# Performance work log

Hardware: AMD Instinct MI355X
Metric: run time of the kernel (lower is better)

## Reference

```python
import jax, jax.numpy as jnp
import numpy as np

DIM = 256
HEADS = 8
NX = NY = 48
RNG = 5
MAX_IDX = (RNG + 1) ** 2  # 36, padding token


def _make_tokens(nx, ny, rng):
    # Half-symmetric tokenization of 2D relative positions (Learnable_rel_pos_embedding.tokenize)
    xm, ym = np.meshgrid(np.arange(nx), np.arange(ny), indexing='ij')
    xm, ym = xm.ravel(), ym.ravel()
    dx = xm[None, :] - xm[:, None]
    dy = ym[None, :] - ym[:, None]
    tok = np.abs(dx) * (rng + 1) + np.abs(dy)
    tok[(np.abs(dx) > rng) | (np.abs(dy) > rng)] = MAX_IDX
    return tok.astype(np.int32)


def setup_inputs() -> dict:
    key = jax.random.key(0)
    ks = jax.random.split(key, 10)
    s = DIM ** -0.5
    x = jax.random.normal(ks[0], (1, DIM, NX, NY), dtype=jnp.float32)
    Wq = jax.random.normal(ks[1], (DIM, DIM), dtype=jnp.float32) * s
    bq = jax.random.normal(ks[2], (DIM,), dtype=jnp.float32) * 0.01
    Wk = jax.random.normal(ks[3], (DIM, DIM), dtype=jnp.float32) * s
    bk = jax.random.normal(ks[4], (DIM,), dtype=jnp.float32) * 0.01
    Wv = jax.random.normal(ks[5], (DIM, DIM), dtype=jnp.float32) * s
    bv = jax.random.normal(ks[6], (DIM,), dtype=jnp.float32) * 0.01
    Wp = jax.random.normal(ks[7], (DIM, DIM), dtype=jnp.float32) * s
    bp = jax.random.normal(ks[8], (DIM,), dtype=jnp.float32) * 0.01
    emb = jax.random.normal(ks[9], (MAX_IDX + 1, HEADS), dtype=jnp.float32) * 0.02
    tokens = jnp.asarray(_make_tokens(NX, NY, RNG))  # (N, N) int32
    return dict(x=x, Wq=Wq, bq=bq, Wk=Wk, bk=bk, Wv=Wv, bv=bv,
                Wp=Wp, bp=bp, emb=emb, tokens=tokens)


def reference(x, Wq, bq, Wk, bk, Wv, bv, Wp, bp, emb, tokens):
    B, C, nx, ny = x.shape
    H = emb.shape[1]
    hd = C // H
    N = nx * ny
    scale = hd ** -0.5

    def conv1x1(W, b, t):
        return (jnp.einsum('oc,bcxy->boxy', W, t) + b[None, :, None, None])

    # Q/K/V as 1x1 convs, split into heads: (B, H, hd, N)
    q = conv1x1(Wq, bq, x).reshape(B, H, hd, N)
    k = conv1x1(Wk, bk, x).reshape(B, H, hd, N)
    v = conv1x1(Wv, bv, x).reshape(B, H, hd, N)

    # attn_method=2: scores = scale*QK^T + relative positional bias
    scores = jnp.einsum('bhdn,bhdm->bhnm', q, k) * scale  # (B, H, N, N)

    # pos_type=5: embedding lookup over half-symmetric relative-position tokens
    pad = emb.shape[0] - 1
    emb_masked = emb.at[pad].set(0.0)  # padding_idx row is zero
    pe = emb_masked[tokens]            # (N, N, H)
    scores = scores + jnp.transpose(pe, (2, 0, 1))[None]

    attn = jax.nn.softmax(scores, axis=-1)
    out = jnp.einsum('bhnm,bhdm->bhdn', attn, v).reshape(B, C, nx, ny)
    out = conv1x1(Wp, bp, out)
    return out
```

## Files before the change

kernel.cpp:

```cpp
#include <hip/hip_runtime.h>

#define NN 2304
#define CC 256
#define HH 8
#define HD 32
#define NYY 48
#define SCALE 0.17677669529663687f

typedef __bf16 bf16_t;
typedef __bf16 bf8v __attribute__((ext_vector_type(8)));
typedef float f4v __attribute__((ext_vector_type(4)));

__device__ __forceinline__ f4v mfma16(bf8v a, bf8v b, f4v c) {
    return __builtin_amdgcn_mfma_f32_16x16x32_bf16(a, b, c, 0, 0, 0);
}

__global__ __launch_bounds__(256) void k_pre(
    const float* __restrict__ x, bf16_t* __restrict__ xT,
    const float* __restrict__ Wq, const float* __restrict__ Wk,
    const float* __restrict__ Wv, const float* __restrict__ Wp,
    bf16_t* __restrict__ Wb) {
    const int b = blockIdx.x;
    const int t = threadIdx.x;
    if (b < 288) {
        __shared__ float tile[64][33];
        const int c0 = (b & 7) * 32;
        const int n0 = (b >> 3) * 64;
        const int n = t & 63, cb = t >> 6;
#pragma unroll
        for (int cc = 0; cc < 8; cc++) {
            int c = cc * 4 + cb;
            tile[n][c] = x[(size_t)(c0 + c) * NN + n0 + n];
        }
        __syncthreads();
        const int c = t & 31, nb = t >> 5;
#pragma unroll
        for (int nn = 0; nn < 8; nn++) {
            int n2 = nn * 8 + nb;
            xT[(size_t)(n0 + n2) * CC + c0 + c] = (bf16_t)tile[n2][c];
        }
    } else {
        const int wb = b - 288;
        const int matid = wb >> 5;
        const float* src = (matid == 0) ? Wq : (matid == 1) ? Wk : (matid == 2) ? Wv : Wp;
        const int base = (wb & 31) * 2048 + t * 8;
        float4 a = *(const float4*)(src + base);
        float4 c = *(const float4*)(src + base + 4);
        bf8v o;
        o[0] = (bf16_t)a.x; o[1] = (bf16_t)a.y; o[2] = (bf16_t)a.z; o[3] = (bf16_t)a.w;
        o[4] = (bf16_t)c.x; o[5] = (bf16_t)c.y; o[6] = (bf16_t)c.z; o[7] = (bf16_t)c.w;
        *(bf8v*)(Wb + (size_t)matid * 65536 + base) = o;
    }
}

__global__ __launch_bounds__(256) void k_proj_qkv(
    const bf16_t* __restrict__ Wb,
    const float* __restrict__ bq, const float* __restrict__ bk,
    const float* __restrict__ bv,
    const bf16_t* __restrict__ xT,
    bf16_t* __restrict__ Qt, bf16_t* __restrict__ Kt, bf16_t* __restrict__ Vd) {
    const int mat = blockIdx.z;
    const bf16_t* W = Wb + (size_t)mat * 65536;
    const float* bias = (mat == 0) ? bq : (mat == 1) ? bk : bv;
    const int n0 = blockIdx.x * 32;
    const int o0 = blockIdx.y * 64;
    const int lane = threadIdx.x & 63;
    const int wave = threadIdx.x >> 6;
    const int l15 = lane & 15;
    const int quad = lane >> 4;
    const int orow = o0 + wave * 16;

    f4v acc0 = {0.f, 0.f, 0.f, 0.f}, acc1 = {0.f, 0.f, 0.f, 0.f};
#pragma unroll
    for (int k0 = 0; k0 < CC; k0 += 32) {
        bf8v af = *(const bf8v*)(W + (size_t)(orow + l15) * CC + k0 + quad * 8);
        bf8v b0 = *(const bf8v*)(xT + (size_t)(n0 + l15) * CC + k0 + quad * 8);
        bf8v b1 = *(const bf8v*)(xT + (size_t)(n0 + 16 + l15) * CC + k0 + quad * 8);
        acc0 = mfma16(af, b0, acc0);
        acc1 = mfma16(af, b1, acc1);
    }

#pragma unroll
    for (int r = 0; r < 4; r++) {
        const int o = orow + quad * 4 + r;
        const float bo = bias[o];
#pragma unroll
        for (int nb = 0; nb < 2; nb++) {
            const int n = n0 + nb * 16 + l15;
            float v = (nb ? acc1[r] : acc0[r]) + bo;
            if (mat == 2) {
                Vd[(size_t)o * NN + n] = (bf16_t)v;
            } else {
                int h = o >> 5, d = o & 31;
                bf16_t* dst = (mat == 0) ? Qt : Kt;
                float vv = (mat == 0) ? v * SCALE : v;
                dst[(size_t)h * NN * HD + (size_t)n * HD + d] = (bf16_t)vv;
            }
        }
    }
}

__global__ __launch_bounds__(256) void k_attn_split(
    const bf16_t* __restrict__ Qt, const bf16_t* __restrict__ Kt,
    const bf16_t* __restrict__ Vd, const float* __restrict__ emb,
    float* __restrict__ pO, float* __restrict__ pl, int L) {
    __shared__ float lds_emb[40];
    __shared__ bf16_t lds_p[4][16 * 32];
    const int h = blockIdx.x & 7;
    const int qt = blockIdx.x >> 3;
    const int sidx = blockIdx.y;
    const int t = threadIdx.x;
    if (t < 37) lds_emb[t] = (t < 36) ? emb[t * HH + h] : 0.0f;
    __syncthreads();

    const int wave = t >> 6, lane = t & 63;
    const int l15 = lane & 15, quad = lane >> 4;
    const int qg0 = qt * 64 + wave * 16;
    const bf16_t* Qh = Qt + (size_t)h * NN * HD;
    const bf16_t* Kh = Kt + (size_t)h * NN * HD;
    const bf16_t* Vh = Vd + (size_t)h * HD * NN;

    const bf8v aq = *(const bf8v*)(Qh + (size_t)(qg0 + l15) * HD + quad * 8);

    int xi[4], yi[4];
#pragma unroll
    for (int r = 0; r < 4; r++) {
        int qi = qg0 + quad * 4 + r;
        xi[r] = qi / NYY;
        yi[r] = qi - xi[r] * NYY;
    }

    f4v o0 = {0.f, 0.f, 0.f, 0.f}, o1 = {0.f, 0.f, 0.f, 0.f};
    const f4v z = {0.f, 0.f, 0.f, 0.f};
    float lsum[4] = {0.f, 0.f, 0.f, 0.f};
    bf16_t* plds = &lds_p[wave][0];

    const int k_begin = sidx * L, k_end = k_begin + L;
    for (int kb = k_begin; kb < k_end; kb += 32) {
        bf8v kf0 = *(const bf8v*)(Kh + (size_t)(kb + l15) * HD + quad * 8);
        bf8v kf1 = *(const bf8v*)(Kh + (size_t)(kb + 16 + l15) * HD + quad * 8);
        bf8v vf0 = *(const bf8v*)(Vh + (size_t)l15 * NN + kb + quad * 8);
        bf8v vf1 = *(const bf8v*)(Vh + (size_t)(16 + l15) * NN + kb + quad * 8);
        f4v s0 = mfma16(aq, kf0, z);
        f4v s1 = mfma16(aq, kf1, z);
#pragma unroll
        for (int cb = 0; cb < 2; cb++) {
            const f4v& s = cb ? s1 : s0;
            int kj = kb + cb * 16 + l15;
            int xj = kj / NYY;
            int yj = kj - xj * NYY;
#pragma unroll
            for (int r = 0; r < 4; r++) {
                int dx = xi[r] - xj; dx = dx < 0 ? -dx : dx;
                int dy = yi[r] - yj; dy = dy < 0 ? -dy : dy;
                int tok = (dx > 5 || dy > 5) ? 36 : dx * 6 + dy;
                float p = __expf(s[r] + lds_emb[tok]);
                lsum[r] += p;
                plds[(quad * 4 + r) * 32 + cb * 16 + l15] = (bf16_t)p;
            }
        }
        bf8v ap = *(const bf8v*)(plds + l15 * 32 + quad * 8);
        o0 = mfma16(ap, vf0, o0);
        o1 = mfma16(ap, vf1, o1);
    }

    float* pO_s = pO + ((size_t)sidx * HH + h) * NN * HD;
    float* pl_s = pl + ((size_t)sidx * HH + h) * NN;
#pragma unroll
    for (int r = 0; r < 4; r++) {
        float v = lsum[r];
#pragma unroll
        for (int m = 1; m < 16; m <<= 1) v += __shfl_xor(v, m, 64);
        int row = qg0 + quad * 4 + r;
        pO_s[(size_t)row * HD + l15] = o0[r];
        pO_s[(size_t)row * HD + 16 + l15] = o1[r];
        if (l15 == 0) pl_s[row] = v;
    }
}

__global__ __launch_bounds__(256) void k_reduce(
    const float* __restrict__ pO, const float* __restrict__ pl,
    bf16_t* __restrict__ Yt, int S) {
    const int e = blockIdx.x * 256 + threadIdx.x;
    const int h = e / (NN * HD);
    const int rem = e - h * (NN * HD);
    const int q = rem >> 5;
    const int d = rem & 31;
    float so = 0.f, sl = 0.f;
    for (int s = 0; s < S; s++) {
        so += pO[((size_t)s * HH + h) * NN * HD + (size_t)q * HD + d];
        sl += pl[((size_t)s * HH + h) * NN + q];
    }
    Yt[(size_t)q * CC + h * HD + d] = (bf16_t)(so / sl);
}

__global__ __launch_bounds__(256) void k_proj_out(
    const bf16_t* __restrict__ Wb, const float* __restrict__ bp,
    const bf16_t* __restrict__ Yt, float* __restrict__ out) {
    const bf16_t* W = Wb + (size_t)3 * 65536;
    const int n0 = blockIdx.x * 32;
    const int o0 = blockIdx.y * 64;
    const int lane = threadIdx.x & 63;
    const int wave = threadIdx.x >> 6;
    const int l15 = lane & 15;
    const int quad = lane >> 4;
    const int orow = o0 + wave * 16;

    f4v acc0 = {0.f, 0.f, 0.f, 0.f}, acc1 = {0.f, 0.f, 0.f, 0.f};
#pragma unroll
    for (int k0 = 0; k0 < CC; k0 += 32) {
        bf8v af = *(const bf8v*)(W + (size_t)(orow + l15) * CC + k0 + quad * 8);
        bf8v b0 = *(const bf8v*)(Yt + (size_t)(n0 + l15) * CC + k0 + quad * 8);
        bf8v b1 = *(const bf8v*)(Yt + (size_t)(n0 + 16 + l15) * CC + k0 + quad * 8);
        acc0 = mfma16(af, b0, acc0);
        acc1 = mfma16(af, b1, acc1);
    }

#pragma unroll
    for (int r = 0; r < 4; r++) {
        const int o = orow + quad * 4 + r;
        const float bo = bp[o];
        out[(size_t)o * NN + n0 + l15] = acc0[r] + bo;
        out[(size_t)o * NN + n0 + 16 + l15] = acc1[r] + bo;
    }
}

extern "C" void kernel_launch(void* const* d_in, const int* in_sizes, int n_in,
                              void* d_out, int out_size, void* d_ws, size_t ws_size,
                              hipStream_t stream) {
    const float* x   = (const float*)d_in[0];
    const float* Wq  = (const float*)d_in[1];
    const float* bq  = (const float*)d_in[2];
    const float* Wk  = (const float*)d_in[3];
    const float* bk  = (const float*)d_in[4];
    const float* Wv  = (const float*)d_in[5];
    const float* bv  = (const float*)d_in[6];
    const float* Wp  = (const float*)d_in[7];
    const float* bp  = (const float*)d_in[8];
    const float* emb = (const float*)d_in[9];
    float* out = (float*)d_out;

    bf16_t* xT = (bf16_t*)d_ws;
    bf16_t* Qt = xT + (size_t)NN * CC;
    bf16_t* Kt = Qt + (size_t)NN * CC;
    bf16_t* Vd = Kt + (size_t)NN * CC;
    bf16_t* Yt = Vd + (size_t)NN * CC;
    bf16_t* Wb = Yt + (size_t)NN * CC;
    float*  pO = (float*)(Wb + (size_t)4 * CC * CC);

    const size_t base_bytes = (size_t)5 * NN * CC * 2 + (size_t)4 * CC * CC * 2;
    const size_t per_split = (size_t)HH * NN * HD * 4 + (size_t)HH * NN * 4;
    int S = 1;
    if (base_bytes + 8 * per_split <= ws_size) S = 8;
    else if (base_bytes + 4 * per_split <= ws_size) S = 4;
    else if (base_bytes + 2 * per_split <= ws_size) S = 2;
    float* pl = pO + (size_t)S * HH * NN * HD;
    const int L = NN / S;

    hipLaunchKernelGGL(k_pre, dim3(288 + 128), dim3(256), 0, stream,
                       x, xT, Wq, Wk, Wv, Wp, Wb);
    hipLaunchKernelGGL(k_proj_qkv, dim3(72, 4, 3), dim3(256), 0, stream,
                       Wb, bq, bk, bv, xT, Qt, Kt, Vd);
    hipLaunchKernelGGL(k_attn_split, dim3(288, S), dim3(256), 0, stream,
                       Qt, Kt, Vd, emb, pO, pl, L);
    hipLaunchKernelGGL(k_reduce, dim3((HH * NN * HD) / 256), dim3(256), 0, stream,
                       pO, pl, Yt, S);
    hipLaunchKernelGGL(k_proj_out, dim3(72, 4), dim3(256), 0, stream, Wb, bp, Yt, out);
}
```

Baseline: 151.1 us.

## Prefetch K/V in attention loop, vectorize reduce, split-K output projection

The attention kernel becomes templated on a compile-time iteration count. It prefetches the next K/V fragments while the current tile computes, tracks key coordinates incrementally instead of dividing per element, and sets an occupancy hint in launch bounds. The reduce kernel now processes four elements per thread with float4 loads and bf16x4 stores. The output projection uses 512 threads, splitting the K dimension across two wave groups and combining them through LDS. The prefetch raises register pressure, and the last iteration does a redundant wrap-around load.

Measured after the change: 154.9 us. +2.5%, slower.

```diff
diff --git a/kernel.cpp b/kernel.cpp
--- a/kernel.cpp
+++ b/kernel.cpp
@@ -9,6 +9,7 @@
 
 typedef __bf16 bf16_t;
 typedef __bf16 bf8v __attribute__((ext_vector_type(8)));
+typedef __bf16 bf4v __attribute__((ext_vector_type(4)));
 typedef float f4v __attribute__((ext_vector_type(4)));
 
 __device__ __forceinline__ f4v mfma16(bf8v a, bf8v b, f4v c) {
@@ -100,10 +101,11 @@
     }
 }
 
-__global__ __launch_bounds__(256) void k_attn_split(
+template <int NITER>
+__global__ __launch_bounds__(256, 8) void k_attn_split(
     const bf16_t* __restrict__ Qt, const bf16_t* __restrict__ Kt,
     const bf16_t* __restrict__ Vd, const float* __restrict__ emb,
-    float* __restrict__ pO, float* __restrict__ pl, int L) {
+    float* __restrict__ pO, float* __restrict__ pl) {
     __shared__ float lds_emb[40];
     __shared__ bf16_t lds_p[4][16 * 32];
     const int h = blockIdx.x & 7;
@@ -130,38 +132,57 @@
         yi[r] = qi - xi[r] * NYY;
     }
 
+    const int k_begin = sidx * (NITER * 32);
+    int kj0 = k_begin + l15;
+    int xj0 = kj0 / NYY, yj0 = kj0 - xj0 * NYY;
+    int yj1 = yj0 + 16, xj1 = xj0;
+    if (yj1 >= NYY) { yj1 -= NYY; xj1++; }
+
     f4v o0 = {0.f, 0.f, 0.f, 0.f}, o1 = {0.f, 0.f, 0.f, 0.f};
     const f4v z = {0.f, 0.f, 0.f, 0.f};
     float lsum[4] = {0.f, 0.f, 0.f, 0.f};
     bf16_t* plds = &lds_p[wave][0];
 
-    const int k_begin = sidx * L, k_end = k_begin + L;
-    for (int kb = k_begin; kb < k_end; kb += 32) {
-        bf8v kf0 = *(const bf8v*)(Kh + (size_t)(kb + l15) * HD + quad * 8);
-        bf8v kf1 = *(const bf8v*)(Kh + (size_t)(kb + 16 + l15) * HD + quad * 8);
-        bf8v vf0 = *(const bf8v*)(Vh + (size_t)l15 * NN + kb + quad * 8);
-        bf8v vf1 = *(const bf8v*)(Vh + (size_t)(16 + l15) * NN + kb + quad * 8);
+    bf8v kf0 = *(const bf8v*)(Kh + (size_t)(k_begin + l15) * HD + quad * 8);
+    bf8v kf1 = *(const bf8v*)(Kh + (size_t)(k_begin + 16 + l15) * HD + quad * 8);
+    bf8v vf0 = *(const bf8v*)(Vh + (size_t)l15 * NN + k_begin + quad * 8);
+    bf8v vf1 = *(const bf8v*)(Vh + (size_t)(16 + l15) * NN + k_begin + quad * 8);
+
+#pragma unroll 1
+    for (int it = 0; it < NITER; ++it) {
+        const int kb = k_begin + it * 32;
+        const int nkb = (it + 1 < NITER) ? kb + 32 : k_begin;
+        bf8v nkf0 = *(const bf8v*)(Kh + (size_t)(nkb + l15) * HD + quad * 8);
+        bf8v nkf1 = *(const bf8v*)(Kh + (size_t)(nkb + 16 + l15) * HD + quad * 8);
+        bf8v nvf0 = *(const bf8v*)(Vh + (size_t)l15 * NN + nkb + quad * 8);
+        bf8v nvf1 = *(const bf8v*)(Vh + (size_t)(16 + l15) * NN + nkb + quad * 8);
+
         f4v s0 = mfma16(aq, kf0, z);
         f4v s1 = mfma16(aq, kf1, z);
 #pragma unroll
-        for (int cb = 0; cb < 2; cb++) {
-            const f4v& s = cb ? s1 : s0;
-            int kj = kb + cb * 16 + l15;
-            int xj = kj / NYY;
-            int yj = kj - xj * NYY;
-#pragma unroll
-            for (int r = 0; r < 4; r++) {
-                int dx = xi[r] - xj; dx = dx < 0 ? -dx : dx;
-                int dy = yi[r] - yj; dy = dy < 0 ? -dy : dy;
-                int tok = (dx > 5 || dy > 5) ? 36 : dx * 6 + dy;
-                float p = __expf(s[r] + lds_emb[tok]);
-                lsum[r] += p;
-                plds[(quad * 4 + r) * 32 + cb * 16 + l15] = (bf16_t)p;
-            }
+        for (int r = 0; r < 4; r++) {
+            int dx = xi[r] - xj0; dx = dx < 0 ? -dx : dx;
+            int dy = yi[r] - yj0; dy = dy < 0 ? -dy : dy;
+            int tok = (dx > 5 || dy > 5) ? 36 : dx * 6 + dy;
+            float p = __expf(s0[r] + lds_emb[tok]);
+            lsum[r] += p;
+            plds[(quad * 4 + r) * 32 + l15] = (bf16_t)p;
+        }
+#pragma unroll
+        for (int r = 0; r < 4; r++) {
+            int dx = xi[r] - xj1; dx = dx < 0 ? -dx : dx;
+            int dy = yi[r] - yj1; dy = dy < 0 ? -dy : dy;
+            int tok = (dx > 5 || dy > 5) ? 36 : dx * 6 + dy;
+            float p = __expf(s1[r] + lds_emb[tok]);
+            lsum[r] += p;
+            plds[(quad * 4 + r) * 32 + 16 + l15] = (bf16_t)p;
         }
         bf8v ap = *(const bf8v*)(plds + l15 * 32 + quad * 8);
         o0 = mfma16(ap, vf0, o0);
         o1 = mfma16(ap, vf1, o1);
+        kf0 = nkf0; kf1 = nkf1; vf0 = nvf0; vf1 = nvf1;
+        yj0 += 32; if (yj0 >= NYY) { yj0 -= NYY; xj0++; }
+        yj1 += 32; if (yj1 >= NYY) { yj1 -= NYY; xj1++; }
     }
 
     float* pO_s = pO + ((size_t)sidx * HH + h) * NN * HD;
@@ -181,34 +202,45 @@
 __global__ __launch_bounds__(256) void k_reduce(
     const float* __restrict__ pO, const float* __restrict__ pl,
     bf16_t* __restrict__ Yt, int S) {
-    const int e = blockIdx.x * 256 + threadIdx.x;
-    const int h = e / (NN * HD);
-    const int rem = e - h * (NN * HD);
-    const int q = rem >> 5;
-    const int d = rem & 31;
-    float so = 0.f, sl = 0.f;
+    const int e4 = blockIdx.x * 256 + threadIdx.x;
+    const int h = e4 / (NN * HD / 4);
+    const int rem = e4 - h * (NN * HD / 4);
+    const int q = rem >> 3;
+    const int d = (rem & 7) * 4;
+    float4 so = {0.f, 0.f, 0.f, 0.f};
+    float sl = 0.f;
     for (int s = 0; s < S; s++) {
-        so += pO[((size_t)s * HH + h) * NN * HD + (size_t)q * HD + d];
+        const float4 v = *(const float4*)(pO + ((size_t)s * HH + h) * NN * HD + (size_t)q * HD + d);
+        so.x += v.x; so.y += v.y; so.z += v.z; so.w += v.w;
         sl += pl[((size_t)s * HH + h) * NN + q];
     }
-    Yt[(size_t)q * CC + h * HD + d] = (bf16_t)(so / sl);
-}
-
-__global__ __launch_bounds__(256) void k_proj_out(
+    const float inv = 1.0f / sl;
+    bf4v o;
+    o[0] = (bf16_t)(so.x * inv); o[1] = (bf16_t)(so.y * inv);
+    o[2] = (bf16_t)(so.z * inv); o[3] = (bf16_t)(so.w * inv);
+    *(bf4v*)(Yt + (size_t)q * CC + h * HD + d) = o;
+}
+
+__global__ __launch_bounds__(512) void k_proj_out(
     const bf16_t* __restrict__ Wb, const float* __restrict__ bp,
     const bf16_t* __restrict__ Yt, float* __restrict__ out) {
+    __shared__ float red[4 * 16 * 32];
     const bf16_t* W = Wb + (size_t)3 * 65536;
     const int n0 = blockIdx.x * 32;
     const int o0 = blockIdx.y * 64;
-    const int lane = threadIdx.x & 63;
-    const int wave = threadIdx.x >> 6;
+    const int t = threadIdx.x;
+    const int lane = t & 63;
+    const int wave = t >> 6;
+    const int og = wave & 3;
+    const int kg = wave >> 2;
     const int l15 = lane & 15;
     const int quad = lane >> 4;
-    const int orow = o0 + wave * 16;
+    const int orow = o0 + og * 16;
 
     f4v acc0 = {0.f, 0.f, 0.f, 0.f}, acc1 = {0.f, 0.f, 0.f, 0.f};
 #pragma unroll
-    for (int k0 = 0; k0 < CC; k0 += 32) {
+    for (int ki = 0; ki < 4; ki++) {
+        const int k0 = kg * 128 + ki * 32;
         bf8v af = *(const bf8v*)(W + (size_t)(orow + l15) * CC + k0 + quad * 8);
         bf8v b0 = *(const bf8v*)(Yt + (size_t)(n0 + l15) * CC + k0 + quad * 8);
         bf8v b1 = *(const bf8v*)(Yt + (size_t)(n0 + 16 + l15) * CC + k0 + quad * 8);
@@ -216,12 +248,25 @@
         acc1 = mfma16(af, b1, acc1);
     }
 
-#pragma unroll
-    for (int r = 0; r < 4; r++) {
-        const int o = orow + quad * 4 + r;
-        const float bo = bp[o];
-        out[(size_t)o * NN + n0 + l15] = acc0[r] + bo;
-        out[(size_t)o * NN + n0 + 16 + l15] = acc1[r] + bo;
+    float* rg = red + og * 512;
+    if (kg == 1) {
+#pragma unroll
+        for (int r = 0; r < 4; r++) {
+            rg[(quad * 4 + r) * 32 + l15] = acc0[r];
+            rg[(quad * 4 + r) * 32 + 16 + l15] = acc1[r];
+        }
+    }
+    __syncthreads();
+    if (kg == 0) {
+#pragma unroll
+        for (int r = 0; r < 4; r++) {
+            const int o = orow + quad * 4 + r;
+            const float bo = bp[o];
+            out[(size_t)o * NN + n0 + l15] =
+                acc0[r] + rg[(quad * 4 + r) * 32 + l15] + bo;
+            out[(size_t)o * NN + n0 + 16 + l15] =
+                acc1[r] + rg[(quad * 4 + r) * 32 + 16 + l15] + bo;
+        }
     }
 }
 
@@ -255,15 +300,18 @@
     else if (base_bytes + 4 * per_split <= ws_size) S = 4;
     else if (base_bytes + 2 * per_split <= ws_size) S = 2;
     float* pl = pO + (size_t)S * HH * NN * HD;
-    const int L = NN / S;
 
     hipLaunchKernelGGL(k_pre, dim3(288 + 128), dim3(256), 0, stream,
                        x, xT, Wq, Wk, Wv, Wp, Wb);
     hipLaunchKernelGGL(k_proj_qkv, dim3(72, 4, 3), dim3(256), 0, stream,
                        Wb, bq, bk, bv, xT, Qt, Kt, Vd);
-    hipLaunchKernelGGL(k_attn_split, dim3(288, S), dim3(256), 0, stream,
-                       Qt, Kt, Vd, emb, pO, pl, L);
-    hipLaunchKernelGGL(k_reduce, dim3((HH * NN * HD) / 256), dim3(256), 0, stream,
+    switch (S) {
+        case 8: hipLaunchKernelGGL((k_attn_split<9>),  dim3(288, 8), dim3(256), 0, stream, Qt, Kt, Vd, emb, pO, pl); break;
+        case 4: hipLaunchKernelGGL((k_attn_split<18>), dim3(288, 4), dim3(256), 0, stream, Qt, Kt, Vd, emb, pO, pl); break;
+        case 2: hipLaunchKernelGGL((k_attn_split<36>), dim3(288, 2), dim3(256), 0, stream, Qt, Kt, Vd, emb, pO, pl); break;
+        default: hipLaunchKernelGGL((k_attn_split<72>), dim3(288, 1), dim3(256), 0, stream, Qt, Kt, Vd, emb, pO, pl); break;
+    }
+    hipLaunchKernelGGL(k_reduce, dim3((HH * NN * HD) / 1024), dim3(256), 0, stream,
                        pO, pl, Yt, S);
-    hipLaunchKernelGGL(k_proj_out, dim3(72, 4), dim3(256), 0, stream, Wb, bp, Yt, out);
-}
+    hipLaunchKernelGGL(k_proj_out, dim3(72, 4), dim3(512), 0, stream, Wb, bp, Yt, out);
+}
```
